# Kernel tuning notes

Measured on AMD Instinct MI355X. Metric: run time of the kernel, lower is better.

Reference implementation:

```python
import jax, jax.numpy as jnp
import numpy as np

N = 100000
E = 1600000
NFEAT, NHID1, NHID2, NCLASS, NSTRUC = 512, 256, 128, 40, 128


def glorot(key, shape):
    lim = 1.0 / np.sqrt(shape[0])
    return jax.random.uniform(key, shape, jnp.float32, -lim, lim)


def setup_inputs() -> dict:
    key = jax.random.key(0)
    ks = jax.random.split(key, 12)
    x = jax.random.normal(ks[0], (N, NFEAT), jnp.float32)
    edge_index = jax.random.randint(ks[1], (2, E), 0, N, jnp.int32)
    edge_weight = jax.random.uniform(ks[2], (E,), jnp.float32)
    return {
        "x": x,
        "edge_index": edge_index,
        "edge_weight": edge_weight,
        "W1": glorot(ks[3], (NFEAT, NHID1)), "b1": jnp.zeros((NHID1,), jnp.float32),
        "W2": glorot(ks[4], (NHID1, NHID2)), "b2": jnp.zeros((NHID2,), jnp.float32),
        "W3": glorot(ks[5], (NHID2, NCLASS)), "b3": jnp.zeros((NCLASS,), jnp.float32),
        "We": glorot(ks[6], (NHID1, NSTRUC)), "be": jnp.zeros((NSTRUC,), jnp.float32),
    }


def spmm(edge_index, edge_weight, support):
    # adj @ support with adj given as weighted edge list (dst <- src)
    src, dst = edge_index[0], edge_index[1]
    msgs = support[src] * edge_weight[:, None]  # [E, d]
    return jax.ops.segment_sum(msgs, dst, num_segments=N)


def gc_layer(x, edge_index, edge_weight, W, b):
    support = x @ W
    return spmm(edge_index, edge_weight, support) + b


def reference(x, edge_index, edge_weight, W1, b1, W2, b2, W3, b3, We, be):
    # eval mode: dropout is identity
    h = jax.nn.relu(gc_layer(x, edge_index, edge_weight, W1, b1))
    out1 = jax.nn.relu(gc_layer(h, edge_index, edge_weight, W2, b2))
    out1 = gc_layer(out1, edge_index, edge_weight, W3, b3)
    out2 = h @ We + be
    return jax.nn.log_softmax(out1, axis=1), out2
```

## Files before the change

kernel.cpp:

```cpp
#include <hip/hip_runtime.h>
#include <hip/hip_bf16.h>

#define NNODES 100000
#define NEDGES 1600000
#define BSH 7
#define NBUCK ((NNODES + 127) >> 7)
#define SPBLK 1536

typedef __attribute__((ext_vector_type(8))) short bf16x8;
typedef __attribute__((ext_vector_type(4))) short bf16x4;
typedef __attribute__((ext_vector_type(2))) short bf16x2;
typedef __attribute__((ext_vector_type(4))) float f32x4;
typedef __attribute__((ext_vector_type(2))) float f32x2;

static __device__ __forceinline__ short f2bf(float f) {
  __hip_bfloat16 b = __float2bfloat16(f);
  return __builtin_bit_cast(short, b);
}
static __device__ __forceinline__ float bf2f(short s) {
  unsigned int u = ((unsigned int)(unsigned short)s) << 16;
  return __builtin_bit_cast(float, u);
}
static __device__ __forceinline__ void fma4(f32x4& a, float w, bf16x4 v) {
  a[0] = fmaf(w, bf2f(v[0]), a[0]);
  a[1] = fmaf(w, bf2f(v[1]), a[1]);
  a[2] = fmaf(w, bf2f(v[2]), a[2]);
  a[3] = fmaf(w, bf2f(v[3]), a[3]);
}
static __device__ __forceinline__ void fma2(f32x2& a, float w, bf16x2 v) {
  a[0] = fmaf(w, bf2f(v[0]), a[0]);
  a[1] = fmaf(w, bf2f(v[1]), a[1]);
}

static __device__ __forceinline__ void gload16(const void* g, void* l) {
  __builtin_amdgcn_global_load_lds(
      (const __attribute__((address_space(1))) unsigned int*)g,
      (__attribute__((address_space(3))) unsigned int*)l, 16, 0, 0);
}

__global__ void wtrans_kernel(const float* __restrict__ W, short* __restrict__ Wt,
                              int K, int Nvalid, int Npad) {
  int idx = blockIdx.x * blockDim.x + threadIdx.x;
  if (idx >= Npad * K) return;
  int n = idx / K, k = idx - n * K;
  int ks = (k & ~63) | ((((k >> 3) & 7) ^ (n & 7)) << 3) | (k & 7);
  Wt[idx] = (n < Nvalid) ? f2bf(W[(size_t)ks * Nvalid + n]) : (short)0;
}

__global__ void bcount_kernel(const int* __restrict__ ei, int* __restrict__ bcnt) {
  __shared__ int h[NBUCK];
  for (int i = threadIdx.x; i < NBUCK; i += 256) h[i] = 0;
  __syncthreads();
  int stride = gridDim.x * 256;
  for (int e = blockIdx.x * 256 + threadIdx.x; e < NEDGES; e += stride)
    atomicAdd(&h[ei[NEDGES + e] >> BSH], 1);
  __syncthreads();
  for (int i = threadIdx.x; i < NBUCK; i += 256)
    if (h[i]) atomicAdd(&bcnt[i], h[i]);
}

__global__ void bscan_kernel(const int* __restrict__ bcnt, int* __restrict__ bbase,
                             int* __restrict__ bcur, int* __restrict__ rowptr) {
  __shared__ int lds[1024];
  int t = threadIdx.x;
  int c = (t < NBUCK) ? bcnt[t] : 0;
  lds[t] = c;
  __syncthreads();
  for (int off = 1; off < 1024; off <<= 1) {
    int v = (t >= off) ? lds[t - off] : 0;
    __syncthreads();
    lds[t] += v;
    __syncthreads();
  }
  if (t < NBUCK) {
    int ex = lds[t] - c;
    bbase[t] = ex;
    bcur[t] = ex;
  }
  if (t == NBUCK) bbase[t] = NEDGES;
  if (t == 0) rowptr[NNODES] = NEDGES;
}

#define P4CHUNK 8192
__global__ void bscatter_kernel(const int* __restrict__ ei, const float* __restrict__ ew,
                                int* __restrict__ bcur, int2* __restrict__ tmp) {
  __shared__ int cnt[NBUCK];
  __shared__ int pos[NBUCK];
  int tid = threadIdx.x;
  for (int i = tid; i < NBUCK; i += 256) cnt[i] = 0;
  __syncthreads();
  int base = blockIdx.x * P4CHUNK;
  int end = base + P4CHUNK;
  if (end > NEDGES) end = NEDGES;
  for (int e = base + tid; e < end; e += 256)
    atomicAdd(&cnt[ei[NEDGES + e] >> BSH], 1);
  __syncthreads();
  for (int i = tid; i < NBUCK; i += 256)
    if (cnt[i]) pos[i] = atomicAdd(&bcur[i], cnt[i]);
  __syncthreads();
  for (int e = base + tid; e < end; e += 256) {
    int d = ei[NEDGES + e];
    int b = d >> BSH;
    int p = atomicAdd(&pos[b], 1);
    tmp[p] = make_int2(ei[e] | ((d & 127) << 17), __float_as_int(ew[e]));
  }
}

__global__ void bsort_kernel(const int* __restrict__ bbase, const int2* __restrict__ tmp,
                             int2* __restrict__ edat, int* __restrict__ rowptr) {
  __shared__ int hist[128];
  __shared__ int cur[128];
  int b = blockIdx.x;
  int tid = threadIdx.x;
  int base = bbase[b], cnt = bbase[b + 1] - base;
  if (tid < 128) hist[tid] = 0;
  __syncthreads();
  for (int i = tid; i < cnt; i += 256)
    atomicAdd(&hist[(tmp[base + i].x >> 17) & 127], 1);
  __syncthreads();
  int c = (tid < 128) ? hist[tid] : 0;
  if (tid < 128) cur[tid] = c;
  __syncthreads();
  for (int off = 1; off < 128; off <<= 1) {
    int v = (tid < 128 && tid >= off) ? cur[tid - off] : 0;
    __syncthreads();
    if (tid < 128) cur[tid] += v;
    __syncthreads();
  }
  if (tid < 128) {
    int ex = cur[tid] - c;
    int node = (b << BSH) + tid;
    if (node < NNODES) rowptr[node] = base + ex;
    cur[tid] = base + ex;
  }
  __syncthreads();
  for (int i = tid; i < cnt; i += 256) {
    int2 r = tmp[base + i];
    int d = (r.x >> 17) & 127;
    int p = atomicAdd(&cur[d], 1);
    edat[p] = make_int2(r.x & 0x1FFFF, r.y);
  }
}

#define LDSTR 72
template <bool AF32, int EPI>
__launch_bounds__(256, 2)
__global__ void gemm_tiled(const void* __restrict__ Aptr, int K,
                           const short* __restrict__ Wt,
                           void* __restrict__ Cp0, float* __restrict__ Cp1,
                           const float* __restrict__ bias, int nvalid, int ldc) {
  __shared__ __align__(16) short As[128 * (AF32 ? LDSTR : 64)];
  __shared__ __align__(16) short Bs[128 * 64];
  int tid = threadIdx.x;
  int lane = tid & 63, wv = tid >> 6;
  int wr = wv >> 1, wc = wv & 1;
  int m0 = blockIdx.y * 128;
  int n0 = blockIdx.x * 128;
  f32x4 acc[4][4];
#pragma unroll
  for (int i = 0; i < 4; i++)
#pragma unroll
    for (int j = 0; j < 4; j++) acc[i][j] = (f32x4){0.f, 0.f, 0.f, 0.f};

  int srow = tid >> 3;
  int scol = (tid & 7) * 8;

  for (int k0 = 0; k0 < K; k0 += 64) {
    if constexpr (AF32) {
#pragma unroll
      for (int p = 0; p < 4; p++) {
        int ml = p * 32 + srow;
        int arow = m0 + ml;
        if (arow >= NNODES) arow = NNODES - 1;
        const float* ap = (const float*)Aptr + (size_t)arow * K + k0 + scol;
        f32x4 a0 = *(const f32x4*)ap;
        f32x4 a1 = *(const f32x4*)(ap + 4);
        bf16x8 av;
#pragma unroll
        for (int j = 0; j < 4; j++) { av[j] = f2bf(a0[j]); av[4 + j] = f2bf(a1[j]); }
        *(bf16x8*)&As[ml * LDSTR + scol] = av;
      }
    } else {
#pragma unroll
      for (int p = 0; p < 4; p++) {
        int row = p * 32 + wv * 8 + (lane >> 3);
        int arow = m0 + row;
        if (arow >= NNODES) arow = NNODES - 1;
        gload16((const short*)Aptr + (size_t)arow * K + k0 + (lane & 7) * 8,
                &As[p * 2048 + wv * 512]);
      }
    }
#pragma unroll
    for (int p = 0; p < 4; p++) {
      int row = p * 32 + wv * 8 + (lane >> 3);
      gload16(Wt + (size_t)(n0 + row) * K + k0 + (lane & 7) * 8,
              &Bs[p * 2048 + wv * 512]);
    }
    __syncthreads();
    int r = lane & 15, quad = lane >> 4;
#pragma unroll
    for (int kk = 0; kk < 64; kk += 32) {
      int csw = (kk + quad * 8) ^ ((r & 7) << 3);
      bf16x8 af[4], bfr[4];
#pragma unroll
      for (int i = 0; i < 4; i++) {
        if constexpr (AF32)
          af[i] = *(const bf16x8*)&As[(wr * 64 + i * 16 + r) * LDSTR + kk + quad * 8];
        else
          af[i] = *(const bf16x8*)&As[((wr * 64 + i * 16 + r) << 6) + csw];
      }
#pragma unroll
      for (int j = 0; j < 4; j++)
        bfr[j] = *(const bf16x8*)&Bs[((wc * 64 + j * 16 + r) << 6) + csw];
#pragma unroll
      for (int i = 0; i < 4; i++)
#pragma unroll
        for (int j = 0; j < 4; j++)
          acc[i][j] = __builtin_amdgcn_mfma_f32_16x16x32_bf16(af[i], bfr[j], acc[i][j], 0, 0, 0);
    }
    __syncthreads();
  }

  int quad = lane >> 4, cl = lane & 15;
#pragma unroll
  for (int i = 0; i < 4; i++) {
    int rowb = m0 + wr * 64 + i * 16 + quad * 4;
#pragma unroll
    for (int rr = 0; rr < 4; rr++) {
      int row = rowb + rr;
      if (row < NNODES) {
#pragma unroll
        for (int j = 0; j < 4; j++) {
          int col = n0 + wc * 64 + j * 16 + cl;
          float v = acc[i][j][rr];
          if (EPI == 0) {
            ((short*)Cp0)[(size_t)row * ldc + col] = f2bf(v);
          } else if (EPI == 1) {
            if (col < nvalid) Cp1[(size_t)row * nvalid + col] = v;
          } else {
            if (col < 128) ((short*)Cp0)[(size_t)row * 128 + col] = f2bf(v);
            else Cp1[(size_t)row * 128 + (col - 128)] = v + bias[col - 128];
          }
        }
      }
    }
  }
}


template <int NE>
static __device__ __forceinline__ void gat1(int2 me, int b, const short* Sc,
                                            f32x4& acc0, f32x4& acc1) {
  int src[NE]; float wt[NE]; bf16x4 v[NE];
#pragma unroll
  for (int j = 0; j < NE; j++) {
    src[j] = __builtin_amdgcn_readlane(me.x, b + j);
    wt[j] = __builtin_bit_cast(float, __builtin_amdgcn_readlane(me.y, b + j));
  }
#pragma unroll
  for (int j = 0; j < NE; j++) v[j] = *(const bf16x4*)(Sc + (size_t)src[j] * 256);
#pragma unroll
  for (int j = 0; j < NE; j++) {
    if (j & 1) fma4(acc1, wt[j], v[j]); else fma4(acc0, wt[j], v[j]);
  }
}

template <int NE>
static __device__ __forceinline__ void gat2(int2 me, int b, const short* Sc,
                                            f32x2& acc0, f32x2& acc1) {
  int src[NE]; float wt[NE]; bf16x2 v[NE];
#pragma unroll
  for (int j = 0; j < NE; j++) {
    src[j] = __builtin_amdgcn_readlane(me.x, b + j);
    wt[j] = __builtin_bit_cast(float, __builtin_amdgcn_readlane(me.y, b + j));
  }
#pragma unroll
  for (int j = 0; j < NE; j++) v[j] = *(const bf16x2*)(Sc + (size_t)src[j] * 128);
#pragma unroll
  for (int j = 0; j < NE; j++) {
    if (j & 1) fma2(acc1, wt[j], v[j]); else fma2(acc0, wt[j], v[j]);
  }
}

template <int NE>
static __device__ __forceinline__ void gat3(int2 me, int b, const float* S3l,
                                            float& acc0, float& acc1) {
  int src[NE]; float wt[NE]; float v[NE];
#pragma unroll
  for (int j = 0; j < NE; j++) {
    src[j] = __builtin_amdgcn_readlane(me.x, b + j);
    wt[j] = __builtin_bit_cast(float, __builtin_amdgcn_readlane(me.y, b + j));
  }
#pragma unroll
  for (int j = 0; j < NE; j++) v[j] = S3l[(size_t)src[j] * 40];
#pragma unroll
  for (int j = 0; j < NE; j++) {
    if (j & 1) acc1 = fmaf(wt[j], v[j], acc1); else acc0 = fmaf(wt[j], v[j], acc0);
  }
}

__launch_bounds__(256, 6)
__global__ void spmm1_kernel(const int* __restrict__ rowptr, const int2* __restrict__ edat,
                             const short* __restrict__ S,
                             const float* __restrict__ bias, short* __restrict__ H) {
  int nw = gridDim.x * 4;
  int wid = blockIdx.x * 4 + (threadIdx.x >> 6);
  int lane = threadIdx.x & 63;
  int c0 = lane * 4;
  const short* Sc = S + c0;
  f32x4 bv = *(const f32x4*)(bias + c0);
  for (int node = wid; node < NNODES; node += nw) {
    f32x4 acc0 = (f32x4){0.f, 0.f, 0.f, 0.f};
    f32x4 acc1 = (f32x4){0.f, 0.f, 0.f, 0.f};
    int beg = rowptr[node], end = rowptr[node + 1];
    for (int w0 = beg; w0 < end; w0 += 64) {
      int wcnt = end - w0;
      if (wcnt > 64) wcnt = 64;
      int2 me = (lane < wcnt) ? edat[w0 + lane] : make_int2(0, 0);
      int g16 = wcnt >> 4, rem = wcnt & 15;
      int b = 0;
      for (int g = 0; g < g16; ++g, b += 16) gat1<16>(me, b, Sc, acc0, acc1);
      if (rem) {
        if (rem > 8) gat1<16>(me, b, Sc, acc0, acc1);
        else gat1<8>(me, b, Sc, acc0, acc1);
      }
    }
    bf16x4 h;
#pragma unroll
    for (int j = 0; j < 4; j++) h[j] = f2bf(fmaxf(acc0[j] + acc1[j] + bv[j], 0.f));
    int c0w = ((lane >> 4) << 6) + ((((lane >> 1) & 7) ^ (node & 7)) << 3) + ((lane & 1) << 2);
    *(bf16x4*)(H + (size_t)node * 256 + c0w) = h;
  }
}

__launch_bounds__(256, 6)
__global__ void spmm2_kernel(const int* __restrict__ rowptr, const int2* __restrict__ edat,
                             const short* __restrict__ S,
                             const float* __restrict__ bias, short* __restrict__ H) {
  int nw = gridDim.x * 4;
  int wid = blockIdx.x * 4 + (threadIdx.x >> 6);
  int lane = threadIdx.x & 63;
  int c0 = lane * 2;
  const short* Sc = S + c0;
  float b0 = bias[c0], b1 = bias[c0 + 1];
  for (int node = wid; node < NNODES; node += nw) {
    f32x2 acc0 = (f32x2){0.f, 0.f};
    f32x2 acc1 = (f32x2){0.f, 0.f};
    int beg = rowptr[node], end = rowptr[node + 1];
    for (int w0 = beg; w0 < end; w0 += 64) {
      int wcnt = end - w0;
      if (wcnt > 64) wcnt = 64;
      int2 me = (lane < wcnt) ? edat[w0 + lane] : make_int2(0, 0);
      int g16 = wcnt >> 4, rem = wcnt & 15;
      int b = 0;
      for (int g = 0; g < g16; ++g, b += 16) gat2<16>(me, b, Sc, acc0, acc1);
      if (rem) {
        if (rem > 8) gat2<16>(me, b, Sc, acc0, acc1);
        else gat2<8>(me, b, Sc, acc0, acc1);
      }
    }
    bf16x2 h;
    h[0] = f2bf(fmaxf(acc0[0] + acc1[0] + b0, 0.f));
    h[1] = f2bf(fmaxf(acc0[1] + acc1[1] + b1, 0.f));
    int c0w = ((lane >> 5) << 6) + ((((lane >> 2) & 7) ^ (node & 7)) << 3) + ((lane & 3) << 1);
    *(bf16x2*)(H + (size_t)node * 128 + c0w) = h;
  }
}

__launch_bounds__(256, 6)
__global__ void spmm3_kernel(const int* __restrict__ rowptr, const int2* __restrict__ edat,
                             const float* __restrict__ S3,
                             const float* __restrict__ b3, float* __restrict__ out1) {
  int nw = gridDim.x * 4;
  int wid = blockIdx.x * 4 + (threadIdx.x >> 6);
  int lane = threadIdx.x & 63;
  bool act = lane < 40;
  const float* S3l = S3 + lane;
  float bl = act ? b3[lane] : 0.f;
  for (int node = wid; node < NNODES; node += nw) {
    float acc0 = 0.f, acc1 = 0.f;
    int beg = rowptr[node], end = rowptr[node + 1];
    for (int w0 = beg; w0 < end; w0 += 64) {
      int wcnt = end - w0;
      if (wcnt > 64) wcnt = 64;
      int2 me = (lane < wcnt) ? edat[w0 + lane] : make_int2(0, 0);
      int g16 = wcnt >> 4, rem = wcnt & 15;
      int b = 0;
      for (int g = 0; g < g16; ++g, b += 16) gat3<16>(me, b, S3l, acc0, acc1);
      if (rem) {
        if (rem > 8) gat3<16>(me, b, S3l, acc0, acc1);
        else gat3<8>(me, b, S3l, acc0, acc1);
      }
    }
    float acc = acc0 + acc1 + bl;
    float v = act ? acc : -__builtin_inff();
    for (int off = 32; off > 0; off >>= 1) v = fmaxf(v, __shfl_xor(v, off));
    float e = act ? expf(acc - v) : 0.f;
    for (int off = 32; off > 0; off >>= 1) e += __shfl_xor(e, off);
    float ls = logf(e);
    if (act) out1[(size_t)node * 40 + lane] = acc - v - ls;
  }
}

extern "C" void kernel_launch(void* const* d_in, const int* in_sizes, int n_in,
                              void* d_out, int out_size, void* d_ws, size_t ws_size,
                              hipStream_t stream) {
  const float* x  = (const float*)d_in[0];
  const int*   ei = (const int*)d_in[1];
  const float* ew = (const float*)d_in[2];
  const float* W1 = (const float*)d_in[3];
  const float* b1 = (const float*)d_in[4];
  const float* W2 = (const float*)d_in[5];
  const float* b2 = (const float*)d_in[6];
  const float* W3 = (const float*)d_in[7];
  const float* b3 = (const float*)d_in[8];
  const float* We = (const float*)d_in[9];
  const float* be = (const float*)d_in[10];
  float* out1 = (float*)d_out;
  float* out2 = (float*)d_out + (size_t)NNODES * 40;

  char* w = (char*)d_ws;
  size_t off = 0;
  auto alloc = [&](size_t bytes) -> char* {
    char* p = w + off;
    off += (bytes + 255) & ~(size_t)255;
    return p;
  };
  int*   rowptr = (int*)alloc((size_t)(NNODES + 1) * 4);
  int*   bcnt   = (int*)alloc((size_t)NBUCK * 4);
  int*   bbase  = (int*)alloc((size_t)(NBUCK + 1) * 4);
  int*   bcur   = (int*)alloc((size_t)NBUCK * 4);
  int2*  edat   = (int2*)alloc((size_t)NEDGES * 8);
  short* Wt1    = (short*)alloc((size_t)256 * 512 * 2);
  short* Wt2e   = (short*)alloc((size_t)256 * 256 * 2);
  short* Wt3    = (short*)alloc((size_t)128 * 128 * 2);
  short* S1bf   = (short*)alloc((size_t)NNODES * 256 * 2);
  short* Hbf    = (short*)alloc((size_t)NNODES * 256 * 2);
  short* S2bf   = (short*)alloc((size_t)NNODES * 128 * 2);
  short* Tbf    = (short*)alloc((size_t)NNODES * 128 * 2);
  float* S3     = (float*)alloc(((size_t)NNODES * 40 + 64) * 4);
  int2*  tmp    = (int2*)S3;

  hipMemsetAsync(bcnt, 0, (size_t)NBUCK * 4, stream);
  bcount_kernel<<<256, 256, 0, stream>>>(ei, bcnt);
  bscan_kernel<<<1, 1024, 0, stream>>>(bcnt, bbase, bcur, rowptr);
  bscatter_kernel<<<(NEDGES + P4CHUNK - 1) / P4CHUNK, 256, 0, stream>>>(ei, ew, bcur, tmp);
  bsort_kernel<<<NBUCK, 256, 0, stream>>>(bbase, tmp, edat, rowptr);

  wtrans_kernel<<<(256 * 512 + 255) / 256, 256, 0, stream>>>(W1, Wt1, 512, 256, 256);
  wtrans_kernel<<<(128 * 256 + 255) / 256, 256, 0, stream>>>(W2, Wt2e, 256, 128, 128);
  wtrans_kernel<<<(128 * 256 + 255) / 256, 256, 0, stream>>>(We, Wt2e + (size_t)128 * 256, 256, 128, 128);
  wtrans_kernel<<<(128 * 128 + 255) / 256, 256, 0, stream>>>(W3, Wt3, 128, 40, 128);

  int gblocks = (NNODES + 127) / 128;

  gemm_tiled<true, 0><<<dim3(2, gblocks), 256, 0, stream>>>(x, 512, Wt1, S1bf, nullptr, nullptr, 256, 256);
  spmm1_kernel<<<SPBLK, 256, 0, stream>>>(rowptr, edat, S1bf, b1, Hbf);
  gemm_tiled<false, 2><<<dim3(2, gblocks), 256, 0, stream>>>(Hbf, 256, Wt2e, S2bf, out2, be, 256, 128);
  spmm2_kernel<<<SPBLK, 256, 0, stream>>>(rowptr, edat, S2bf, b2, Tbf);
  gemm_tiled<false, 1><<<dim3(1, gblocks), 256, 0, stream>>>(Tbf, 128, Wt3, nullptr, S3, nullptr, 40, 40);
  spmm3_kernel<<<SPBLK, 256, 0, stream>>>(rowptr, edat, S3, b3, out1);
}
```

Measured before the change: 734.1 us.

## Split wave across edges with 16-byte gathers in SpMM layers 1 and 2

Reworks the layer-1 and layer-2 sparse aggregation so each lane loads 8 bf16 values (16 bytes) per edge instead of 4 or 2. The wave is split into 2 or 4 sub-groups, each handling a different edge and fetching it via ds_bpermute, with partial sums combined by cross-lane shuffles at the end. The aim is wider, fewer memory transactions and more edges in flight per instruction. In exchange it adds bpermute/LDS traffic, shuffle reductions, idle lanes when edge counts are small, and lower occupancy (launch bounds 6 down to 4).

```diff
diff --git a/kernel.cpp b/kernel.cpp
--- a/kernel.cpp
+++ b/kernel.cpp
@@ -21,15 +21,15 @@
   unsigned int u = ((unsigned int)(unsigned short)s) << 16;
   return __builtin_bit_cast(float, u);
 }
-static __device__ __forceinline__ void fma4(f32x4& a, float w, bf16x4 v) {
-  a[0] = fmaf(w, bf2f(v[0]), a[0]);
-  a[1] = fmaf(w, bf2f(v[1]), a[1]);
-  a[2] = fmaf(w, bf2f(v[2]), a[2]);
-  a[3] = fmaf(w, bf2f(v[3]), a[3]);
-}
-static __device__ __forceinline__ void fma2(f32x2& a, float w, bf16x2 v) {
-  a[0] = fmaf(w, bf2f(v[0]), a[0]);
-  a[1] = fmaf(w, bf2f(v[1]), a[1]);
+static __device__ __forceinline__ void fma8(f32x4& lo, f32x4& hi, float w, bf16x8 v) {
+  lo[0] = fmaf(w, bf2f(v[0]), lo[0]);
+  lo[1] = fmaf(w, bf2f(v[1]), lo[1]);
+  lo[2] = fmaf(w, bf2f(v[2]), lo[2]);
+  lo[3] = fmaf(w, bf2f(v[3]), lo[3]);
+  hi[0] = fmaf(w, bf2f(v[4]), hi[0]);
+  hi[1] = fmaf(w, bf2f(v[5]), hi[1]);
+  hi[2] = fmaf(w, bf2f(v[6]), hi[2]);
+  hi[3] = fmaf(w, bf2f(v[7]), hi[3]);
 }
 
 static __device__ __forceinline__ void gload16(const void* g, void* l) {
@@ -249,37 +249,37 @@
 
 
 template <int NE>
-static __device__ __forceinline__ void gat1(int2 me, int b, const short* Sc,
-                                            f32x4& acc0, f32x4& acc1) {
-  int src[NE]; float wt[NE]; bf16x4 v[NE];
+static __device__ __forceinline__ void pgat1(int2 me, int b, int idx0, const short* Sc,
+                                             f32x4* acc) {
+  int s[NE]; float wt[NE]; bf16x8 v[NE];
 #pragma unroll
   for (int j = 0; j < NE; j++) {
-    src[j] = __builtin_amdgcn_readlane(me.x, b + j);
-    wt[j] = __builtin_bit_cast(float, __builtin_amdgcn_readlane(me.y, b + j));
-  }
-#pragma unroll
-  for (int j = 0; j < NE; j++) v[j] = *(const bf16x4*)(Sc + (size_t)src[j] * 256);
+    int idx = idx0 + ((b + 2 * j) << 2);
+    s[j] = __builtin_amdgcn_ds_bpermute(idx, me.x);
+    wt[j] = __builtin_bit_cast(float, __builtin_amdgcn_ds_bpermute(idx, me.y));
+  }
+#pragma unroll
+  for (int j = 0; j < NE; j++) v[j] = *(const bf16x8*)(Sc + (size_t)s[j] * 256);
+#pragma unroll
+  for (int j = 0; j < NE; j++)
+    fma8(acc[(j & 1) * 2], acc[(j & 1) * 2 + 1], wt[j], v[j]);
+}
+
+template <int NE>
+static __device__ __forceinline__ void pgat2(int2 me, int b, int idx0, const short* Sc,
+                                             f32x4* acc) {
+  int s[NE]; float wt[NE]; bf16x8 v[NE];
 #pragma unroll
   for (int j = 0; j < NE; j++) {
-    if (j & 1) fma4(acc1, wt[j], v[j]); else fma4(acc0, wt[j], v[j]);
-  }
-}
-
-template <int NE>
-static __device__ __forceinline__ void gat2(int2 me, int b, const short* Sc,
-                                            f32x2& acc0, f32x2& acc1) {
-  int src[NE]; float wt[NE]; bf16x2 v[NE];
-#pragma unroll
-  for (int j = 0; j < NE; j++) {
-    src[j] = __builtin_amdgcn_readlane(me.x, b + j);
-    wt[j] = __builtin_bit_cast(float, __builtin_amdgcn_readlane(me.y, b + j));
-  }
-#pragma unroll
-  for (int j = 0; j < NE; j++) v[j] = *(const bf16x2*)(Sc + (size_t)src[j] * 128);
-#pragma unroll
-  for (int j = 0; j < NE; j++) {
-    if (j & 1) fma2(acc1, wt[j], v[j]); else fma2(acc0, wt[j], v[j]);
-  }
+    int idx = idx0 + ((b + 4 * j) << 2);
+    s[j] = __builtin_amdgcn_ds_bpermute(idx, me.x);
+    wt[j] = __builtin_bit_cast(float, __builtin_amdgcn_ds_bpermute(idx, me.y));
+  }
+#pragma unroll
+  for (int j = 0; j < NE; j++) v[j] = *(const bf16x8*)(Sc + (size_t)s[j] * 128);
+#pragma unroll
+  for (int j = 0; j < NE; j++)
+    fma8(acc[(j & 1) * 2], acc[(j & 1) * 2 + 1], wt[j], v[j]);
 }
 
 template <int NE>
@@ -299,71 +299,105 @@
   }
 }
 
-__launch_bounds__(256, 6)
+__launch_bounds__(256, 4)
 __global__ void spmm1_kernel(const int* __restrict__ rowptr, const int2* __restrict__ edat,
                              const short* __restrict__ S,
                              const float* __restrict__ bias, short* __restrict__ H) {
   int nw = gridDim.x * 4;
   int wid = blockIdx.x * 4 + (threadIdx.x >> 6);
   int lane = threadIdx.x & 63;
-  int c0 = lane * 4;
-  const short* Sc = S + c0;
-  f32x4 bv = *(const f32x4*)(bias + c0);
+  int half = lane >> 5, sub = lane & 31;
+  int idx0 = half << 2;
+  const short* Sc = S + sub * 8;
+  f32x4 bv0 = *(const f32x4*)(bias + sub * 8);
+  f32x4 bv1 = *(const f32x4*)(bias + sub * 8 + 4);
   for (int node = wid; node < NNODES; node += nw) {
-    f32x4 acc0 = (f32x4){0.f, 0.f, 0.f, 0.f};
-    f32x4 acc1 = (f32x4){0.f, 0.f, 0.f, 0.f};
+    f32x4 acc[4];
+#pragma unroll
+    for (int i = 0; i < 4; i++) acc[i] = (f32x4){0.f, 0.f, 0.f, 0.f};
     int beg = rowptr[node], end = rowptr[node + 1];
     for (int w0 = beg; w0 < end; w0 += 64) {
       int wcnt = end - w0;
       if (wcnt > 64) wcnt = 64;
       int2 me = (lane < wcnt) ? edat[w0 + lane] : make_int2(0, 0);
-      int g16 = wcnt >> 4, rem = wcnt & 15;
-      int b = 0;
-      for (int g = 0; g < g16; ++g, b += 16) gat1<16>(me, b, Sc, acc0, acc1);
-      if (rem) {
-        if (rem > 8) gat1<16>(me, b, Sc, acc0, acc1);
-        else gat1<8>(me, b, Sc, acc0, acc1);
-      }
-    }
-    bf16x4 h;
-#pragma unroll
-    for (int j = 0; j < 4; j++) h[j] = f2bf(fmaxf(acc0[j] + acc1[j] + bv[j], 0.f));
-    int c0w = ((lane >> 4) << 6) + ((((lane >> 1) & 7) ^ (node & 7)) << 3) + ((lane & 1) << 2);
-    *(bf16x4*)(H + (size_t)node * 256 + c0w) = h;
-  }
-}
-
-__launch_bounds__(256, 6)
+      int left = wcnt, b = 0;
+      while (left >= 16) { pgat1<8>(me, b, idx0, Sc, acc); b += 16; left -= 16; }
+      if (left > 8) pgat1<8>(me, b, idx0, Sc, acc);
+      else if (left > 4) pgat1<4>(me, b, idx0, Sc, acc);
+      else if (left > 2) pgat1<2>(me, b, idx0, Sc, acc);
+      else if (left > 0) pgat1<1>(me, b, idx0, Sc, acc);
+    }
+    f32x4 lo, hi;
+#pragma unroll
+    for (int i = 0; i < 4; i++) {
+      lo[i] = acc[0][i] + acc[2][i];
+      hi[i] = acc[1][i] + acc[3][i];
+      lo[i] += __shfl_xor(lo[i], 32);
+      hi[i] += __shfl_xor(hi[i], 32);
+    }
+    if (half == 0) {
+      bf16x8 h;
+#pragma unroll
+      for (int j = 0; j < 4; j++) {
+        h[j] = f2bf(fmaxf(lo[j] + bv0[j], 0.f));
+        h[4 + j] = f2bf(fmaxf(hi[j] + bv1[j], 0.f));
+      }
+      int t = sub >> 3, q = sub & 7;
+      int off = t * 64 + ((q ^ (node & 7)) << 3);
+      *(bf16x8*)(H + (size_t)node * 256 + off) = h;
+    }
+  }
+}
+
+__launch_bounds__(256, 4)
 __global__ void spmm2_kernel(const int* __restrict__ rowptr, const int2* __restrict__ edat,
                              const short* __restrict__ S,
                              const float* __restrict__ bias, short* __restrict__ H) {
   int nw = gridDim.x * 4;
   int wid = blockIdx.x * 4 + (threadIdx.x >> 6);
   int lane = threadIdx.x & 63;
-  int c0 = lane * 2;
-  const short* Sc = S + c0;
-  float b0 = bias[c0], b1 = bias[c0 + 1];
+  int q4 = lane >> 4, sub = lane & 15;
+  int idx0 = q4 << 2;
+  const short* Sc = S + sub * 8;
+  f32x4 bv0 = *(const f32x4*)(bias + sub * 8);
+  f32x4 bv1 = *(const f32x4*)(bias + sub * 8 + 4);
   for (int node = wid; node < NNODES; node += nw) {
-    f32x2 acc0 = (f32x2){0.f, 0.f};
-    f32x2 acc1 = (f32x2){0.f, 0.f};
+    f32x4 acc[4];
+#pragma unroll
+    for (int i = 0; i < 4; i++) acc[i] = (f32x4){0.f, 0.f, 0.f, 0.f};
     int beg = rowptr[node], end = rowptr[node + 1];
     for (int w0 = beg; w0 < end; w0 += 64) {
       int wcnt = end - w0;
       if (wcnt > 64) wcnt = 64;
       int2 me = (lane < wcnt) ? edat[w0 + lane] : make_int2(0, 0);
-      int g16 = wcnt >> 4, rem = wcnt & 15;
-      int b = 0;
-      for (int g = 0; g < g16; ++g, b += 16) gat2<16>(me, b, Sc, acc0, acc1);
-      if (rem) {
-        if (rem > 8) gat2<16>(me, b, Sc, acc0, acc1);
-        else gat2<8>(me, b, Sc, acc0, acc1);
-      }
-    }
-    bf16x2 h;
-    h[0] = f2bf(fmaxf(acc0[0] + acc1[0] + b0, 0.f));
-    h[1] = f2bf(fmaxf(acc0[1] + acc1[1] + b1, 0.f));
-    int c0w = ((lane >> 5) << 6) + ((((lane >> 2) & 7) ^ (node & 7)) << 3) + ((lane & 3) << 1);
-    *(bf16x2*)(H + (size_t)node * 128 + c0w) = h;
+      int left = wcnt, b = 0;
+      while (left >= 32) { pgat2<8>(me, b, idx0, Sc, acc); b += 32; left -= 32; }
+      if (left > 16) pgat2<8>(me, b, idx0, Sc, acc);
+      else if (left > 8) pgat2<4>(me, b, idx0, Sc, acc);
+      else if (left > 4) pgat2<2>(me, b, idx0, Sc, acc);
+      else if (left > 0) pgat2<1>(me, b, idx0, Sc, acc);
+    }
+    f32x4 lo, hi;
+#pragma unroll
+    for (int i = 0; i < 4; i++) {
+      lo[i] = acc[0][i] + acc[2][i];
+      hi[i] = acc[1][i] + acc[3][i];
+      lo[i] += __shfl_xor(lo[i], 32);
+      hi[i] += __shfl_xor(hi[i], 32);
+      lo[i] += __shfl_xor(lo[i], 16);
+      hi[i] += __shfl_xor(hi[i], 16);
+    }
+    if (q4 == 0) {
+      bf16x8 h;
+#pragma unroll
+      for (int j = 0; j < 4; j++) {
+        h[j] = f2bf(fmaxf(lo[j] + bv0[j], 0.f));
+        h[4 + j] = f2bf(fmaxf(hi[j] + bv1[j], 0.f));
+      }
+      int t = sub >> 3, q = sub & 7;
+      int off = t * 64 + ((q ^ (node & 7)) << 3);
+      *(bf16x8*)(H + (size_t)node * 128 + off) = h;
+    }
   }
 }
 
```

Result: no change. 744.4 us (+1.4%).

## Fuse graph preprocessing kernels with first GEMM to overlap independent work

Applied to the files above, without the earlier changes.

Merges the bucket-count and weight-transpose kernels into one front kernel, then splits the first dense GEMM (x @ W1) across two launches that also run the edge scatter and per-bucket sort blocks. The independent GEMM tiles share a grid with the sorting work, which is meant to fill the GPU during the latency-bound preprocessing phases and cut launch count. The cost is larger LDS per block in the fused kernels, which can lower occupancy for the scatter and sort blocks, and block scheduling order now decides how much actually overlaps.

```diff
diff --git a/kernel.cpp b/kernel.cpp
--- a/kernel.cpp
+++ b/kernel.cpp
@@ -6,6 +6,9 @@
 #define BSH 7
 #define NBUCK ((NNODES + 127) >> 7)
 #define SPBLK 1536
+#define P4CHUNK 8192
+#define NSCAT ((NEDGES + P4CHUNK - 1) / P4CHUNK)
+#define MH1 391
 
 typedef __attribute__((ext_vector_type(8))) short bf16x8;
 typedef __attribute__((ext_vector_type(4))) short bf16x4;
@@ -38,25 +41,86 @@
       (__attribute__((address_space(3))) unsigned int*)l, 16, 0, 0);
 }
 
-__global__ void wtrans_kernel(const float* __restrict__ W, short* __restrict__ Wt,
-                              int K, int Nvalid, int Npad) {
-  int idx = blockIdx.x * blockDim.x + threadIdx.x;
+static __device__ __forceinline__ void wtrans_body(int blk, const float* __restrict__ W,
+                                                   short* __restrict__ Wt,
+                                                   int K, int Nvalid, int Npad) {
+  int idx = blk * 256 + threadIdx.x;
   if (idx >= Npad * K) return;
   int n = idx / K, k = idx - n * K;
   int ks = (k & ~63) | ((((k >> 3) & 7) ^ (n & 7)) << 3) | (k & 7);
   Wt[idx] = (n < Nvalid) ? f2bf(W[(size_t)ks * Nvalid + n]) : (short)0;
 }
 
-__global__ void bcount_kernel(const int* __restrict__ ei, int* __restrict__ bcnt) {
-  __shared__ int h[NBUCK];
+static __device__ __forceinline__ void bcount_body(int blk, const int* __restrict__ ei,
+                                                   int* __restrict__ bcnt, int* h) {
   for (int i = threadIdx.x; i < NBUCK; i += 256) h[i] = 0;
   __syncthreads();
-  int stride = gridDim.x * 256;
-  for (int e = blockIdx.x * 256 + threadIdx.x; e < NEDGES; e += stride)
+  for (int e = blk * 256 + threadIdx.x; e < NEDGES; e += 256 * 256)
     atomicAdd(&h[ei[NEDGES + e] >> BSH], 1);
   __syncthreads();
   for (int i = threadIdx.x; i < NBUCK; i += 256)
     if (h[i]) atomicAdd(&bcnt[i], h[i]);
+}
+
+static __device__ __forceinline__ void bscatter_body(int blk, int* cnt, int* pos,
+                                                     const int* __restrict__ ei,
+                                                     const float* __restrict__ ew,
+                                                     int* __restrict__ bcur,
+                                                     int2* __restrict__ tmp) {
+  int tid = threadIdx.x;
+  for (int i = tid; i < NBUCK; i += 256) cnt[i] = 0;
+  __syncthreads();
+  int base = blk * P4CHUNK;
+  int end = base + P4CHUNK;
+  if (end > NEDGES) end = NEDGES;
+  for (int e = base + tid; e < end; e += 256)
+    atomicAdd(&cnt[ei[NEDGES + e] >> BSH], 1);
+  __syncthreads();
+  for (int i = tid; i < NBUCK; i += 256)
+    if (cnt[i]) pos[i] = atomicAdd(&bcur[i], cnt[i]);
+  __syncthreads();
+  for (int e = base + tid; e < end; e += 256) {
+    int d = ei[NEDGES + e];
+    int b = d >> BSH;
+    int p = atomicAdd(&pos[b], 1);
+    tmp[p] = make_int2(ei[e] | ((d & 127) << 17), __float_as_int(ew[e]));
+  }
+}
+
+static __device__ __forceinline__ void bsort_body(int b, int* hist, int* cur,
+                                                  const int* __restrict__ bbase,
+                                                  const int2* __restrict__ tmp,
+                                                  int2* __restrict__ edat,
+                                                  int* __restrict__ rowptr) {
+  int tid = threadIdx.x;
+  int base = bbase[b], cnt = bbase[b + 1] - base;
+  if (tid < 128) hist[tid] = 0;
+  __syncthreads();
+  for (int i = tid; i < cnt; i += 256)
+    atomicAdd(&hist[(tmp[base + i].x >> 17) & 127], 1);
+  __syncthreads();
+  int c = (tid < 128) ? hist[tid] : 0;
+  if (tid < 128) cur[tid] = c;
+  __syncthreads();
+  for (int off = 1; off < 128; off <<= 1) {
+    int v = (tid < 128 && tid >= off) ? cur[tid - off] : 0;
+    __syncthreads();
+    if (tid < 128) cur[tid] += v;
+    __syncthreads();
+  }
+  if (tid < 128) {
+    int ex = cur[tid] - c;
+    int node = (b << BSH) + tid;
+    if (node < NNODES) rowptr[node] = base + ex;
+    cur[tid] = base + ex;
+  }
+  __syncthreads();
+  for (int i = tid; i < cnt; i += 256) {
+    int2 r = tmp[base + i];
+    int d = (r.x >> 17) & 127;
+    int p = atomicAdd(&cur[d], 1);
+    edat[p] = make_int2(r.x & 0x1FFFF, r.y);
+  }
 }
 
 __global__ void bscan_kernel(const int* __restrict__ bcnt, int* __restrict__ bbase,
@@ -81,81 +145,18 @@
   if (t == 0) rowptr[NNODES] = NEDGES;
 }
 
-#define P4CHUNK 8192
-__global__ void bscatter_kernel(const int* __restrict__ ei, const float* __restrict__ ew,
-                                int* __restrict__ bcur, int2* __restrict__ tmp) {
-  __shared__ int cnt[NBUCK];
-  __shared__ int pos[NBUCK];
-  int tid = threadIdx.x;
-  for (int i = tid; i < NBUCK; i += 256) cnt[i] = 0;
-  __syncthreads();
-  int base = blockIdx.x * P4CHUNK;
-  int end = base + P4CHUNK;
-  if (end > NEDGES) end = NEDGES;
-  for (int e = base + tid; e < end; e += 256)
-    atomicAdd(&cnt[ei[NEDGES + e] >> BSH], 1);
-  __syncthreads();
-  for (int i = tid; i < NBUCK; i += 256)
-    if (cnt[i]) pos[i] = atomicAdd(&bcur[i], cnt[i]);
-  __syncthreads();
-  for (int e = base + tid; e < end; e += 256) {
-    int d = ei[NEDGES + e];
-    int b = d >> BSH;
-    int p = atomicAdd(&pos[b], 1);
-    tmp[p] = make_int2(ei[e] | ((d & 127) << 17), __float_as_int(ew[e]));
-  }
-}
-
-__global__ void bsort_kernel(const int* __restrict__ bbase, const int2* __restrict__ tmp,
-                             int2* __restrict__ edat, int* __restrict__ rowptr) {
-  __shared__ int hist[128];
-  __shared__ int cur[128];
-  int b = blockIdx.x;
-  int tid = threadIdx.x;
-  int base = bbase[b], cnt = bbase[b + 1] - base;
-  if (tid < 128) hist[tid] = 0;
-  __syncthreads();
-  for (int i = tid; i < cnt; i += 256)
-    atomicAdd(&hist[(tmp[base + i].x >> 17) & 127], 1);
-  __syncthreads();
-  int c = (tid < 128) ? hist[tid] : 0;
-  if (tid < 128) cur[tid] = c;
-  __syncthreads();
-  for (int off = 1; off < 128; off <<= 1) {
-    int v = (tid < 128 && tid >= off) ? cur[tid - off] : 0;
-    __syncthreads();
-    if (tid < 128) cur[tid] += v;
-    __syncthreads();
-  }
-  if (tid < 128) {
-    int ex = cur[tid] - c;
-    int node = (b << BSH) + tid;
-    if (node < NNODES) rowptr[node] = base + ex;
-    cur[tid] = base + ex;
-  }
-  __syncthreads();
-  for (int i = tid; i < cnt; i += 256) {
-    int2 r = tmp[base + i];
-    int d = (r.x >> 17) & 127;
-    int p = atomicAdd(&cur[d], 1);
-    edat[p] = make_int2(r.x & 0x1FFFF, r.y);
-  }
-}
-
 #define LDSTR 72
 template <bool AF32, int EPI>
-__launch_bounds__(256, 2)
-__global__ void gemm_tiled(const void* __restrict__ Aptr, int K,
-                           const short* __restrict__ Wt,
-                           void* __restrict__ Cp0, float* __restrict__ Cp1,
-                           const float* __restrict__ bias, int nvalid, int ldc) {
-  __shared__ __align__(16) short As[128 * (AF32 ? LDSTR : 64)];
-  __shared__ __align__(16) short Bs[128 * 64];
+static __device__ void gemm_body(int my, int nx, short* As, short* Bs,
+                                 const void* __restrict__ Aptr, int K,
+                                 const short* __restrict__ Wt,
+                                 void* __restrict__ Cp0, float* __restrict__ Cp1,
+                                 const float* __restrict__ bias, int nvalid, int ldc) {
   int tid = threadIdx.x;
   int lane = tid & 63, wv = tid >> 6;
   int wr = wv >> 1, wc = wv & 1;
-  int m0 = blockIdx.y * 128;
-  int n0 = blockIdx.x * 128;
+  int m0 = my * 128;
+  int n0 = nx * 128;
   f32x4 acc[4][4];
 #pragma unroll
   for (int i = 0; i < 4; i++)
@@ -244,6 +245,71 @@
         }
       }
     }
+  }
+}
+
+template <bool AF32, int EPI>
+__launch_bounds__(256, 2)
+__global__ void gemm_tiled(const void* __restrict__ Aptr, int K,
+                           const short* __restrict__ Wt,
+                           void* __restrict__ Cp0, float* __restrict__ Cp1,
+                           const float* __restrict__ bias, int nvalid, int ldc) {
+  __shared__ __align__(16) short As[128 * (AF32 ? LDSTR : 64)];
+  __shared__ __align__(16) short Bs[128 * 64];
+  gemm_body<AF32, EPI>(blockIdx.y, blockIdx.x, As, Bs, Aptr, K, Wt, Cp0, Cp1, bias, nvalid, ldc);
+}
+
+__launch_bounds__(256)
+__global__ void front_kernel(const float* __restrict__ W1, short* __restrict__ Wt1,
+                             const float* __restrict__ W2, const float* __restrict__ We,
+                             short* __restrict__ Wt2e, const float* __restrict__ W3,
+                             short* __restrict__ Wt3,
+                             const int* __restrict__ ei, int* __restrict__ bcnt) {
+  __shared__ int h[NBUCK];
+  int b = blockIdx.x;
+  if (b < 256) { bcount_body(b, ei, bcnt, h); return; }
+  b -= 256;
+  if (b < 512) { wtrans_body(b, W1, Wt1, 512, 256, 256); return; }
+  b -= 512;
+  if (b < 128) { wtrans_body(b, W2, Wt2e, 256, 128, 128); return; }
+  b -= 128;
+  if (b < 128) { wtrans_body(b, We, Wt2e + (size_t)128 * 256, 256, 128, 128); return; }
+  b -= 128;
+  wtrans_body(b, W3, Wt3, 128, 40, 128);
+}
+#define FRONT_BLOCKS (256 + 512 + 128 + 128 + 64)
+
+__launch_bounds__(256, 2)
+__global__ void fuseA_kernel(const int* __restrict__ ei, const float* __restrict__ ew,
+                             int* __restrict__ bcur, int2* __restrict__ tmp,
+                             const float* __restrict__ x, const short* __restrict__ Wt1,
+                             short* __restrict__ S1bf) {
+  __shared__ __align__(16) short As[128 * LDSTR];
+  __shared__ __align__(16) short Bs[128 * 64];
+  __shared__ int sc_cnt[NBUCK];
+  __shared__ int sc_pos[NBUCK];
+  if (blockIdx.x < NSCAT) {
+    bscatter_body(blockIdx.x, sc_cnt, sc_pos, ei, ew, bcur, tmp);
+  } else {
+    int g = blockIdx.x - NSCAT;
+    gemm_body<true, 0>(g >> 1, g & 1, As, Bs, x, 512, Wt1, S1bf, nullptr, nullptr, 256, 256);
+  }
+}
+
+__launch_bounds__(256, 2)
+__global__ void fuseB_kernel(const int* __restrict__ bbase, const int2* __restrict__ tmp,
+                             int2* __restrict__ edat, int* __restrict__ rowptr,
+                             const float* __restrict__ x, const short* __restrict__ Wt1,
+                             short* __restrict__ S1bf) {
+  __shared__ __align__(16) short As[128 * LDSTR];
+  __shared__ __align__(16) short Bs[128 * 64];
+  __shared__ int so_hist[128];
+  __shared__ int so_cur[128];
+  if (blockIdx.x < NBUCK) {
+    bsort_body(blockIdx.x, so_hist, so_cur, bbase, tmp, edat, rowptr);
+  } else {
+    int g = blockIdx.x - NBUCK;
+    gemm_body<true, 0>(MH1 + (g >> 1), g & 1, As, Bs, x, 512, Wt1, S1bf, nullptr, nullptr, 256, 256);
   }
 }
 
@@ -442,19 +508,14 @@
   int2*  tmp    = (int2*)S3;
 
   hipMemsetAsync(bcnt, 0, (size_t)NBUCK * 4, stream);
-  bcount_kernel<<<256, 256, 0, stream>>>(ei, bcnt);
+  front_kernel<<<FRONT_BLOCKS, 256, 0, stream>>>(W1, Wt1, W2, We, Wt2e, W3, Wt3, ei, bcnt);
   bscan_kernel<<<1, 1024, 0, stream>>>(bcnt, bbase, bcur, rowptr);
-  bscatter_kernel<<<(NEDGES + P4CHUNK - 1) / P4CHUNK, 256, 0, stream>>>(ei, ew, bcur, tmp);
-  bsort_kernel<<<NBUCK, 256, 0, stream>>>(bbase, tmp, edat, rowptr);
-
-  wtrans_kernel<<<(256 * 512 + 255) / 256, 256, 0, stream>>>(W1, Wt1, 512, 256, 256);
-  wtrans_kernel<<<(128 * 256 + 255) / 256, 256, 0, stream>>>(W2, Wt2e, 256, 128, 128);
-  wtrans_kernel<<<(128 * 256 + 255) / 256, 256, 0, stream>>>(We, Wt2e + (size_t)128 * 256, 256, 128, 128);
-  wtrans_kernel<<<(128 * 128 + 255) / 256, 256, 0, stream>>>(W3, Wt3, 128, 40, 128);
+
+  fuseA_kernel<<<NSCAT + MH1 * 2, 256, 0, stream>>>(ei, ew, bcur, tmp, x, Wt1, S1bf);
+  fuseB_kernel<<<NBUCK + (782 - MH1) * 2, 256, 0, stream>>>(bbase, tmp, edat, rowptr, x, Wt1, S1bf);
 
   int gblocks = (NNODES + 127) / 128;
 
-  gemm_tiled<true, 0><<<dim3(2, gblocks), 256, 0, stream>>>(x, 512, Wt1, S1bf, nullptr, nullptr, 256, 256);
   spmm1_kernel<<<SPBLK, 256, 0, stream>>>(rowptr, edat, S1bf, b1, Hbf);
   gemm_tiled<false, 2><<<dim3(2, gblocks), 256, 0, stream>>>(Hbf, 256, Wt2e, S2bf, out2, be, 256, 128);
   spmm2_kernel<<<SPBLK, 256, 0, stream>>>(rowptr, edat, S2bf, b2, Tbf);
```

Result: faster. 712.3 us (-3.0%).
